# Kernel optimization log

Hardware: AMD Instinct MI355X
Metric: run time of the kernel (lower is better)

Reference implementation:

```python
import jax, jax.numpy as jnp
import numpy as np

K = 3            # pairwise_size
DIL = 2          # pairwise_dilation
COLOR_THR = 0.3  # pairwise_color_thresh
WARMUP = 1.0     # warmup factor (iter >= pairwise_warmup_iters)
COST_CLASS = 1.0
COST_PROJ = 1.0
COST_PAIR = 1.0


def unfold_wo_center(x, k, d):
    # x: (N, T, H, W) -> (N, T, k*k-1, H, W); neighbor at offset (i,j) with dilation d,
    # zero padding, center (i=j=k//2) removed, row-major order (matches F.unfold).
    pad = d * (k - 1) // 2
    H, W = x.shape[-2:]
    xp = jnp.pad(x, ((0, 0), (0, 0), (pad, pad), (pad, pad)))
    outs = []
    for i in range(k):
        for j in range(k):
            if i == k // 2 and j == k // 2:
                continue
            outs.append(xp[..., i * d:i * d + H, j * d:j * d + W])
    return jnp.stack(outs, axis=2)


def batch_dice_loss(inputs, targets):
    # inputs: (N, C), targets: (M, C)
    numerator = 2.0 * jnp.einsum('nc,mc->nm', inputs, targets)
    denominator = inputs.sum(-1)[:, None] + targets.sum(-1)[None, :]
    return 1.0 - (numerator + 1.0) / (denominator + 1.0)


def batch_axis_projection(out_mask, tgt_box_mask, axis):
    # max-project predicted (sigmoid) and box masks along `axis`, dice between projections
    src = jax.nn.sigmoid(out_mask).max(axis=axis).reshape(out_mask.shape[0], -1)
    tgt = tgt_box_mask.max(axis=axis).reshape(tgt_box_mask.shape[0], -1)
    return batch_dice_loss(src, tgt)


def calculate_similarity_cost_video(out_mask, tgt_box_mask, tgt_similarities):
    # out_mask: (Q,T,H,W); tgt_box_mask: (G,T,H,W); tgt_similarities: (G,T,8,H,W)
    Q, T = out_mask.shape[:2]
    G = tgt_box_mask.shape[0]
    tgt_sim = (tgt_similarities >= COLOR_THR).astype(jnp.float32) * tgt_box_mask[:, :, None]
    log_fg = jax.nn.log_sigmoid(out_mask)
    log_bg = jax.nn.log_sigmoid(-out_mask)
    log_fg_u = unfold_wo_center(log_fg, K, DIL)   # (Q,T,8,H,W)
    log_bg_u = unfold_wo_center(log_bg, K, DIL)
    # -log(exp(fg+fg_u) + exp(bg+bg_u)) computed stably
    src_sim = -jnp.logaddexp(log_fg[:, :, None] + log_fg_u,
                             log_bg[:, :, None] + log_bg_u)  # (Q,T,8,H,W)
    src_flat = src_sim.reshape(Q, T, -1)
    tgt_flat = tgt_sim.reshape(G, T, -1)
    numerator = jnp.einsum('qtc,gtc->tqg', src_flat, tgt_flat)      # (T,Q,G)
    denominator = jnp.clip(tgt_flat.sum(-1), 1.0, None)             # (G,T)
    cost = numerator / denominator.T[:, None, :]                    # (T,Q,G)
    return cost.mean(axis=0)                                        # (Q,G)


def setup_inputs() -> dict:
    key = jax.random.key(0)
    k1, k2, k3, k4, k5 = jax.random.split(key, 5)
    Q, G, T, H, W, C = 100, 16, 2, 128, 128, 81
    return {
        'pred_logits': jax.random.normal(k1, (Q, C), dtype=jnp.float32),
        'out_mask': jax.random.normal(k2, (Q, T, H, W), dtype=jnp.float32),
        'tgt_similarities': jax.random.uniform(k3, (G, T, K * K - 1, H, W), dtype=jnp.float32),
        'tgt_ids': jax.random.randint(k4, (G,), 0, C, dtype=jnp.int32),
        'tgt_box_mask': jax.random.randint(k5, (G, T, H, W), 0, 2, dtype=jnp.int32),
    }


def reference(pred_logits, out_mask, tgt_similarities, tgt_ids, tgt_box_mask):
    tgt_box_f = tgt_box_mask.astype(jnp.float32)
    out_prob = jax.nn.softmax(pred_logits, axis=-1)
    cost_class = -out_prob[:, tgt_ids]                                  # (Q,G)
    cost_projection = (batch_axis_projection(out_mask, tgt_box_f, 3)
                       + batch_axis_projection(out_mask, tgt_box_f, 2))  # (Q,G)
    cost_pairwise = calculate_similarity_cost_video(out_mask, tgt_box_f, tgt_similarities) * WARMUP
    C = COST_CLASS * cost_class + COST_PROJ * cost_projection + COST_PAIR * cost_pairwise
    return C
```

## Files before the change

kernel.cpp:

```cpp
#include <hip/hip_runtime.h>
#include <hip/hip_fp16.h>
#include <cstdint>

#define Q_ 100
#define G_ 16
#define T_ 2
#define H_ 128
#define W_ 128
#define HW_ (H_*W_)
#define C_ 81
#define RS_ 69
#define QS_ 553

typedef _Float16 half8 __attribute__((ext_vector_type(8)));
typedef float floatx4 __attribute__((ext_vector_type(4)));

__device__ __forceinline__ float sig_(float x) { return 1.0f / (1.0f + __expf(-x)); }

__launch_bounds__(256)
__global__ void k_srcmax(const float* __restrict__ om,
                         float* __restrict__ srcMW,
                         float* __restrict__ srcMHp) {
    int qt = blockIdx.x >> 2;
    int rg = blockIdx.x & 3;
    const float* base = om + (size_t)qt * HW_ + rg * 32 * W_;
    int tid = threadIdx.x;

    {
        int r = tid >> 3, seg = tid & 7;
        const float4* rp = (const float4*)(base + r * W_ + seg * 16);
        float m = -1e30f;
        #pragma unroll
        for (int i = 0; i < 4; ++i) {
            float4 v = rp[i];
            m = fmaxf(m, fmaxf(fmaxf(v.x, v.y), fmaxf(v.z, v.w)));
        }
        m = fmaxf(m, __shfl_xor(m, 1, 64));
        m = fmaxf(m, __shfl_xor(m, 2, 64));
        m = fmaxf(m, __shfl_xor(m, 4, 64));
        if (seg == 0) srcMW[qt * 128 + rg * 32 + r] = m;
    }
    __shared__ float cred[128];
    {
        int c = tid & 127, rh = tid >> 7;
        const float* cp = base + rh * 16 * W_ + c;
        float m = -1e30f;
        #pragma unroll
        for (int i = 0; i < 16; ++i) m = fmaxf(m, cp[i * W_]);
        if (rh == 1) cred[c] = m;
        __syncthreads();
        if (rh == 0) srcMHp[(qt * 4 + rg) * 128 + c] = fmaxf(m, cred[c]);
    }
}

__launch_bounds__(256)
__global__ void k_tgtmax(const int* __restrict__ box,
                         int* __restrict__ tgtMWi,
                         int* __restrict__ tgtMHp) {
    int gt = blockIdx.x >> 3;
    int rg = blockIdx.x & 7;
    const int* base = box + (size_t)gt * HW_ + rg * 16 * W_;
    int tid = threadIdx.x;
    {
        int r = tid >> 4, seg = tid & 15;
        const int4* rp = (const int4*)(base + r * W_ + seg * 8);
        int4 a = rp[0], b = rp[1];
        int m = max(max(max(a.x, a.y), max(a.z, a.w)),
                    max(max(b.x, b.y), max(b.z, b.w)));
        m = max(m, __shfl_xor(m, 1, 64));
        m = max(m, __shfl_xor(m, 2, 64));
        m = max(m, __shfl_xor(m, 4, 64));
        m = max(m, __shfl_xor(m, 8, 64));
        if (seg == 0) tgtMWi[gt * 128 + rg * 16 + r] = m;
    }
    __shared__ int credi[128];
    {
        int c = tid & 127, rh = tid >> 7;
        const int* cp = base + rh * 8 * W_ + c;
        int m = 0;
        #pragma unroll
        for (int i = 0; i < 8; ++i) m = max(m, cp[i * W_]);
        if (rh == 1) credi[c] = m;
        __syncthreads();
        if (rh == 0) tgtMHp[(gt * 8 + rg) * 128 + c] = max(m, credi[c]);
    }
}

__launch_bounds__(256)
__global__ void k_pack(const float* __restrict__ sims,
                       const int* __restrict__ box,
                       uint32_t* __restrict__ packed,
                       int* __restrict__ cnt_part) {
    int bid = blockIdx.x;
    int gg = bid & 3;
    int pxblk = bid >> 2;
    int tid = threadIdx.x;
    int p0 = pxblk * 512 + tid * 2;
    int t = p0 >> 14;
    int pp = p0 & (HW_ - 1);

    uint32_t w0 = 0, w1 = 0;
    int pc[4];
    #pragma unroll
    for (int b = 0; b < 4; ++b) {
        int g = gg * 4 + b;
        const float* sbase = sims + ((size_t)(g * T_ + t) * 8) * HW_ + pp;
        int2 bx = *(const int2*)(box + (size_t)(g * T_ + t) * HW_ + pp);
        uint32_t by0 = 0, by1 = 0;
        #pragma unroll
        for (int e = 0; e < 8; ++e) {
            float2 sv = *(const float2*)(sbase + (size_t)e * HW_);
            by0 |= (sv.x >= 0.3f ? 1u : 0u) << e;
            by1 |= (sv.y >= 0.3f ? 1u : 0u) << e;
        }
        by0 = bx.x ? by0 : 0u;
        by1 = bx.y ? by1 : 0u;
        w0 |= by0 << (b * 8);
        w1 |= by1 << (b * 8);
        pc[b] = __popc(by0) + __popc(by1);
    }
    *(uint2*)&packed[(size_t)gg * (T_ * HW_) + p0] = make_uint2(w0, w1);

    __shared__ int redI[4][4];
    int wid = tid >> 6, lane = tid & 63;
    #pragma unroll
    for (int b = 0; b < 4; ++b) {
        int s = pc[b];
        #pragma unroll
        for (int o = 32; o > 0; o >>= 1) s += __shfl_down(s, o, 64);
        if (lane == 0) redI[wid][b] = s;
    }
    __syncthreads();
    if (tid < 4)
        cnt_part[pxblk * 16 + gg * 4 + tid] =
            redI[0][tid] + redI[1][tid] + redI[2][tid] + redI[3][tid];
}

__global__ void k_dice(const float* __restrict__ logits, const int* __restrict__ ids,
                       const float* __restrict__ srcMW, const float* __restrict__ srcMHp,
                       const int* __restrict__ tgtMWi, const int* __restrict__ tgtMHp,
                       const int* __restrict__ cnt_part,
                       int* __restrict__ cntF,
                       float* __restrict__ out) {
    int q = blockIdx.x >> 4;
    int g = blockIdx.x & 15;
    int l = threadIdx.x;

    if (q == 0) {
        int tt = l >> 5, pb = l & 31;
        int v = cnt_part[(tt * 32 + pb) * 16 + g];
        #pragma unroll
        for (int o = 1; o <= 16; o <<= 1) v += __shfl_xor(v, o, 64);
        if (pb == 0) cntF[tt * G_ + g] = v;
    }

    float v0 = (l < C_) ? logits[q * C_ + l] : -1e30f;
    float v1 = (l + 64 < C_) ? logits[q * C_ + l + 64] : -1e30f;
    float mx = fmaxf(v0, v1);
    #pragma unroll
    for (int o = 32; o > 0; o >>= 1) mx = fmaxf(mx, __shfl_xor(mx, o, 64));
    float es = ((l < C_) ? __expf(v0 - mx) : 0.0f)
             + ((l + 64 < C_) ? __expf(v1 - mx) : 0.0f);
    #pragma unroll
    for (int o = 32; o > 0; o >>= 1) es += __shfl_xor(es, o, 64);

    float d3 = 0, t3 = 0, s3 = 0, d2 = 0, t2 = 0, s2 = 0;
    #pragma unroll
    for (int i = 0; i < 4; ++i) {
        int c = i * 64 + l;
        int tt = c >> 7, cc = c & 127;
        float sW = sig_(srcMW[(q * 2 + tt) * 128 + cc]);
        float mh = srcMHp[((q * 2 + tt) * 4 + 0) * 128 + cc];
        #pragma unroll
        for (int r = 1; r < 4; ++r)
            mh = fmaxf(mh, srcMHp[((q * 2 + tt) * 4 + r) * 128 + cc]);
        float sH = sig_(mh);
        float tW = (float)tgtMWi[(g * 2 + tt) * 128 + cc];
        int th = tgtMHp[((g * 2 + tt) * 8 + 0) * 128 + cc];
        #pragma unroll
        for (int r = 1; r < 8; ++r)
            th = max(th, tgtMHp[((g * 2 + tt) * 8 + r) * 128 + cc]);
        float tH = (float)th;
        d3 += sW * tW; t3 += tW; s3 += sW;
        d2 += sH * tH; t2 += tH; s2 += sH;
    }
    #pragma unroll
    for (int o = 32; o > 0; o >>= 1) {
        d3 += __shfl_xor(d3, o, 64); t3 += __shfl_xor(t3, o, 64);
        s3 += __shfl_xor(s3, o, 64); d2 += __shfl_xor(d2, o, 64);
        t2 += __shfl_xor(t2, o, 64); s2 += __shfl_xor(s2, o, 64);
    }
    if (l == 0) {
        float p = __expf(logits[q * C_ + ids[g]] - mx) / es;
        float dice3 = 1.0f - (2.0f * d3 + 1.0f) / (s3 + t3 + 1.0f);
        float dice2 = 1.0f - (2.0f * d2 + 1.0f) / (s2 + t2 + 1.0f);
        out[q * G_ + g] = -p + dice3 + dice2;
    }
}

__launch_bounds__(256, 4)
__global__ void k_pair(const float* __restrict__ om,
                       const uint32_t* __restrict__ packed,
                       const int* __restrict__ cntF,
                       float* __restrict__ out) {
    int bid = blockIdx.x;
    int wh = bid & 1;
    int rg = (bid >> 1) & 31;
    int t  = (bid >> 6) & 1;
    int qt = bid >> 7;
    int qbase = qt * 16;
    int rowbase = rg * 4;
    int cbase = wh * 64;
    int tid = threadIdx.x;

    __shared__ uint32_t tile[16 * QS_];

    #pragma unroll
    for (int i = 0; i < 8; ++i) {
        int idx = i * 256 + tid;
        int c4 = idx & 15;
        int row = (idx >> 4) & 7;
        int q = idx >> 7;
        int gq = qbase + q;
        int grow = rowbase - 2 + row;
        float4 x = make_float4(0.f, 0.f, 0.f, 0.f);
        if (gq < Q_ && (unsigned)grow < (unsigned)H_)
            x = *(const float4*)(om + (((size_t)gq * T_ + t) * H_ + grow) * W_ + cbase + c4 * 4);
        uint32_t* dst = &tile[q * QS_ + row * RS_ + 2 + c4 * 4];
        {
            float E = __expf(-x.x); __half2 h = __floats2half2_rn(E, __logf(1.f + E)); dst[0] = *(uint32_t*)&h;
        }{
            float E = __expf(-x.y); __half2 h = __floats2half2_rn(E, __logf(1.f + E)); dst[1] = *(uint32_t*)&h;
        }{
            float E = __expf(-x.z); __half2 h = __floats2half2_rn(E, __logf(1.f + E)); dst[2] = *(uint32_t*)&h;
        }{
            float E = __expf(-x.w); __half2 h = __floats2half2_rn(E, __logf(1.f + E)); dst[3] = *(uint32_t*)&h;
        }
    }
    #pragma unroll
    for (int i = 0; i < 2; ++i) {
        int idx = i * 256 + tid;
        int cc = idx & 3;
        int row = (idx >> 2) & 7;
        int q = idx >> 5;
        int col = (cc < 2) ? cc : cc + 64;
        int gcol = cbase - 2 + col;
        int gq = qbase + q;
        int grow = rowbase - 2 + row;
        float x = 0.f;
        if (gq < Q_ && (unsigned)grow < (unsigned)H_ && (unsigned)gcol < (unsigned)W_)
            x = om[(((size_t)gq * T_ + t) * H_ + grow) * W_ + gcol];
        float E = __expf(-x);
        __half2 h = __floats2half2_rn(E, __logf(1.f + E));
        tile[q * QS_ + row * RS_ + col] = *(uint32_t*)&h;
    }
    __syncthreads();

    int l = tid & 63;
    int w = tid >> 6;
    int mn = l & 15;
    int pq = l >> 4;
    int growS = rowbase + w;

    const uint32_t* pbase = packed + (size_t)(mn >> 2) * (T_ * HW_) + t * HW_
                          + (growS << 7) + cbase + (pq << 4);
    uint4 pkA = *(const uint4*)(pbase + 0);
    uint4 pkB = *(const uint4*)(pbase + 4);
    uint4 pkC = *(const uint4*)(pbase + 8);
    uint4 pkD = *(const uint4*)(pbase + 12);
    uint32_t pkw[16] = {pkA.x, pkA.y, pkA.z, pkA.w, pkB.x, pkB.y, pkB.z, pkB.w,
                        pkC.x, pkC.y, pkC.z, pkC.w, pkD.x, pkD.y, pkD.z, pkD.w};

    const uint32_t* tq = &tile[mn * QS_ + (w + 2) * RS_ + 2 + (pq << 4)];

    bool rowU = (growS >= 2), rowD = (growS <= H_ - 3);
    int bsh = (mn & 3) * 8;

    const int dy[8] = {-2,-2,-2, 0,0, 2,2,2};
    const int dx[8] = {-2, 0, 2,-2,2,-2,0,2};

    floatx4 acc0 = {0.f,0.f,0.f,0.f}, acc1 = {0.f,0.f,0.f,0.f};

    #pragma unroll
    for (int grp = 0; grp < 16; ++grp) {
        int gcol = cbase + (pq << 4) + grp;
        bool colL = (gcol >= 2), colR = (gcol <= W_ - 3);
        bool m8[8] = {rowU && colL, rowU, rowU && colR,
                      colL, colR,
                      rowD && colL, rowD, rowD && colR};

        uint32_t selfw = tq[grp];
        __half2 sh = *(__half2*)&selfw;
        float Ep = __half2float(__low2half(sh));
        float Lp = __half2float(__high2half(sh));
        uint32_t byte = (pkw[grp] >> bsh) & 255u;

        half8 af, bf;
        #pragma unroll
        for (int e = 0; e < 8; ++e) {
            uint32_t nw = tq[grp + dy[e] * RS_ + dx[e]];
            __half2 nh = *(__half2*)&nw;
            float En = __half2float(__low2half(nh));
            float Ln = __half2float(__high2half(nh));
            float s = Lp + Ln - __logf(fmaf(Ep, En, 1.0f));
            s = m8[e] ? s : 0.0f;
            af[e] = (_Float16)s;
            bf[e] = (_Float16)(float)((byte >> e) & 1u);
        }
        if (grp & 1) acc1 = __builtin_amdgcn_mfma_f32_16x16x32_f16(af, bf, acc1, 0, 0, 0);
        else         acc0 = __builtin_amdgcn_mfma_f32_16x16x32_f16(af, bf, acc0, 0, 0, 0);
    }

    __syncthreads();
    float* red = (float*)tile;
    #pragma unroll
    for (int j = 0; j < 4; ++j)
        red[(w * 16 + pq * 4 + j) * 17 + mn] = acc0[j] + acc1[j];
    __syncthreads();
    {
        int row = tid >> 4, g = tid & 15;
        float v = red[(0 * 16 + row) * 17 + g] + red[(1 * 16 + row) * 17 + g]
                + red[(2 * 16 + row) * 17 + g] + red[(3 * 16 + row) * 17 + g];
        int gq = qbase + row;
        if (gq < Q_) {
            int den = max(1, cntF[t * G_ + g]);
            atomicAdd(&out[gq * G_ + g], v * (0.5f / (float)den));
        }
    }
}

extern "C" void kernel_launch(void* const* d_in, const int* in_sizes, int n_in,
                              void* d_out, int out_size, void* d_ws, size_t ws_size,
                              hipStream_t stream) {
    const float* pred_logits = (const float*)d_in[0];
    const float* out_mask    = (const float*)d_in[1];
    const float* sims        = (const float*)d_in[2];
    const int*   tgt_ids     = (const int*)d_in[3];
    const int*   tgt_box     = (const int*)d_in[4];
    float* out = (float*)d_out;

    float*    srcMW    = (float*)d_ws;
    float*    srcMHp   = srcMW + Q_ * T_ * 128;
    int*      tgtMWi   = (int*)(srcMHp + Q_ * T_ * 4 * 128);
    int*      tgtMHp   = tgtMWi + G_ * T_ * 128;
    int*      cnt_part = tgtMHp + G_ * T_ * 8 * 128;
    int*      cntF     = cnt_part + 64 * 16;
    uint32_t* packed   = (uint32_t*)(cntF + G_ * T_);

    k_srcmax<<<Q_ * T_ * 4, 256, 0, stream>>>(out_mask, srcMW, srcMHp);
    k_tgtmax<<<G_ * T_ * 8, 256, 0, stream>>>(tgt_box, tgtMWi, tgtMHp);
    k_pack<<<(T_ * HW_ / 512) * 4, 256, 0, stream>>>(sims, tgt_box, packed, cnt_part);
    k_dice<<<Q_ * G_, 64, 0, stream>>>(pred_logits, tgt_ids, srcMW, srcMHp,
                                       tgtMWi, tgtMHp, cnt_part, cntF, out);
    k_pair<<<7 * T_ * 32 * 2, 256, 0, stream>>>(out_mask, packed, cntF, out);
}
```

Before: 122.2 us.

## Merge three prep kernels into one launch and build MFMA B operand via bit tricks

Merges k_srcmax, k_tgtmax and k_pack into a single k_prep kernel that dispatches on block index ranges. This removes two kernel launches and lets the independent prep work overlap across CUs. Separately, in k_pair the 0/1 half-precision B operand is now built with integer bit tricks (multiplying the isolated bits by the fp16 encoding of 1.0) instead of per-element int-to-float-to-half conversions. Shared memory is reused across the branches; the merged kernel keeps the same per-branch work.

```diff
diff --git a/kernel.cpp b/kernel.cpp
--- a/kernel.cpp
+++ b/kernel.cpp
@@ -18,122 +18,119 @@
 __device__ __forceinline__ float sig_(float x) { return 1.0f / (1.0f + __expf(-x)); }
 
 __launch_bounds__(256)
-__global__ void k_srcmax(const float* __restrict__ om,
-                         float* __restrict__ srcMW,
-                         float* __restrict__ srcMHp) {
-    int qt = blockIdx.x >> 2;
-    int rg = blockIdx.x & 3;
-    const float* base = om + (size_t)qt * HW_ + rg * 32 * W_;
-    int tid = threadIdx.x;
-
-    {
-        int r = tid >> 3, seg = tid & 7;
-        const float4* rp = (const float4*)(base + r * W_ + seg * 16);
-        float m = -1e30f;
-        #pragma unroll
-        for (int i = 0; i < 4; ++i) {
-            float4 v = rp[i];
-            m = fmaxf(m, fmaxf(fmaxf(v.x, v.y), fmaxf(v.z, v.w)));
-        }
-        m = fmaxf(m, __shfl_xor(m, 1, 64));
-        m = fmaxf(m, __shfl_xor(m, 2, 64));
-        m = fmaxf(m, __shfl_xor(m, 4, 64));
-        if (seg == 0) srcMW[qt * 128 + rg * 32 + r] = m;
-    }
-    __shared__ float cred[128];
-    {
-        int c = tid & 127, rh = tid >> 7;
-        const float* cp = base + rh * 16 * W_ + c;
-        float m = -1e30f;
-        #pragma unroll
-        for (int i = 0; i < 16; ++i) m = fmaxf(m, cp[i * W_]);
-        if (rh == 1) cred[c] = m;
-        __syncthreads();
-        if (rh == 0) srcMHp[(qt * 4 + rg) * 128 + c] = fmaxf(m, cred[c]);
-    }
-}
-
-__launch_bounds__(256)
-__global__ void k_tgtmax(const int* __restrict__ box,
-                         int* __restrict__ tgtMWi,
-                         int* __restrict__ tgtMHp) {
-    int gt = blockIdx.x >> 3;
-    int rg = blockIdx.x & 7;
-    const int* base = box + (size_t)gt * HW_ + rg * 16 * W_;
-    int tid = threadIdx.x;
-    {
-        int r = tid >> 4, seg = tid & 15;
-        const int4* rp = (const int4*)(base + r * W_ + seg * 8);
-        int4 a = rp[0], b = rp[1];
-        int m = max(max(max(a.x, a.y), max(a.z, a.w)),
-                    max(max(b.x, b.y), max(b.z, b.w)));
-        m = max(m, __shfl_xor(m, 1, 64));
-        m = max(m, __shfl_xor(m, 2, 64));
-        m = max(m, __shfl_xor(m, 4, 64));
-        m = max(m, __shfl_xor(m, 8, 64));
-        if (seg == 0) tgtMWi[gt * 128 + rg * 16 + r] = m;
-    }
-    __shared__ int credi[128];
-    {
-        int c = tid & 127, rh = tid >> 7;
-        const int* cp = base + rh * 8 * W_ + c;
-        int m = 0;
-        #pragma unroll
-        for (int i = 0; i < 8; ++i) m = max(m, cp[i * W_]);
-        if (rh == 1) credi[c] = m;
-        __syncthreads();
-        if (rh == 0) tgtMHp[(gt * 8 + rg) * 128 + c] = max(m, credi[c]);
-    }
-}
-
-__launch_bounds__(256)
-__global__ void k_pack(const float* __restrict__ sims,
+__global__ void k_prep(const float* __restrict__ om,
                        const int* __restrict__ box,
+                       const float* __restrict__ sims,
+                       float* __restrict__ srcMW,
+                       float* __restrict__ srcMHp,
+                       int* __restrict__ tgtMWi,
+                       int* __restrict__ tgtMHp,
                        uint32_t* __restrict__ packed,
                        int* __restrict__ cnt_part) {
+    __shared__ float credF[128];
+    __shared__ int redI[4][4];
     int bid = blockIdx.x;
-    int gg = bid & 3;
-    int pxblk = bid >> 2;
     int tid = threadIdx.x;
-    int p0 = pxblk * 512 + tid * 2;
-    int t = p0 >> 14;
-    int pp = p0 & (HW_ - 1);
-
-    uint32_t w0 = 0, w1 = 0;
-    int pc[4];
-    #pragma unroll
-    for (int b = 0; b < 4; ++b) {
-        int g = gg * 4 + b;
-        const float* sbase = sims + ((size_t)(g * T_ + t) * 8) * HW_ + pp;
-        int2 bx = *(const int2*)(box + (size_t)(g * T_ + t) * HW_ + pp);
-        uint32_t by0 = 0, by1 = 0;
-        #pragma unroll
-        for (int e = 0; e < 8; ++e) {
-            float2 sv = *(const float2*)(sbase + (size_t)e * HW_);
-            by0 |= (sv.x >= 0.3f ? 1u : 0u) << e;
-            by1 |= (sv.y >= 0.3f ? 1u : 0u) << e;
-        }
-        by0 = bx.x ? by0 : 0u;
-        by1 = bx.y ? by1 : 0u;
-        w0 |= by0 << (b * 8);
-        w1 |= by1 << (b * 8);
-        pc[b] = __popc(by0) + __popc(by1);
-    }
-    *(uint2*)&packed[(size_t)gg * (T_ * HW_) + p0] = make_uint2(w0, w1);
-
-    __shared__ int redI[4][4];
-    int wid = tid >> 6, lane = tid & 63;
-    #pragma unroll
-    for (int b = 0; b < 4; ++b) {
-        int s = pc[b];
-        #pragma unroll
-        for (int o = 32; o > 0; o >>= 1) s += __shfl_down(s, o, 64);
-        if (lane == 0) redI[wid][b] = s;
-    }
-    __syncthreads();
-    if (tid < 4)
-        cnt_part[pxblk * 16 + gg * 4 + tid] =
-            redI[0][tid] + redI[1][tid] + redI[2][tid] + redI[3][tid];
+
+    if (bid < 800) {
+        int qt = bid >> 2;
+        int rg = bid & 3;
+        const float* base = om + (size_t)qt * HW_ + rg * 32 * W_;
+        {
+            int r = tid >> 3, seg = tid & 7;
+            const float4* rp = (const float4*)(base + r * W_ + seg * 16);
+            float m = -1e30f;
+            #pragma unroll
+            for (int i = 0; i < 4; ++i) {
+                float4 v = rp[i];
+                m = fmaxf(m, fmaxf(fmaxf(v.x, v.y), fmaxf(v.z, v.w)));
+            }
+            m = fmaxf(m, __shfl_xor(m, 1, 64));
+            m = fmaxf(m, __shfl_xor(m, 2, 64));
+            m = fmaxf(m, __shfl_xor(m, 4, 64));
+            if (seg == 0) srcMW[qt * 128 + rg * 32 + r] = m;
+        }
+        {
+            int c = tid & 127, rh = tid >> 7;
+            const float* cp = base + rh * 16 * W_ + c;
+            float m = -1e30f;
+            #pragma unroll
+            for (int i = 0; i < 16; ++i) m = fmaxf(m, cp[i * W_]);
+            if (rh == 1) credF[c] = m;
+            __syncthreads();
+            if (rh == 0) srcMHp[(qt * 4 + rg) * 128 + c] = fmaxf(m, credF[c]);
+        }
+    } else if (bid < 1056) {
+        int b2 = bid - 800;
+        int gt = b2 >> 3;
+        int rg = b2 & 7;
+        const int* base = box + (size_t)gt * HW_ + rg * 16 * W_;
+        {
+            int r = tid >> 4, seg = tid & 15;
+            const int4* rp = (const int4*)(base + r * W_ + seg * 8);
+            int4 a = rp[0], b = rp[1];
+            int m = max(max(max(a.x, a.y), max(a.z, a.w)),
+                        max(max(b.x, b.y), max(b.z, b.w)));
+            m = max(m, __shfl_xor(m, 1, 64));
+            m = max(m, __shfl_xor(m, 2, 64));
+            m = max(m, __shfl_xor(m, 4, 64));
+            m = max(m, __shfl_xor(m, 8, 64));
+            if (seg == 0) tgtMWi[gt * 128 + rg * 16 + r] = m;
+        }
+        {
+            int* credi = (int*)credF;
+            int c = tid & 127, rh = tid >> 7;
+            const int* cp = base + rh * 8 * W_ + c;
+            int m = 0;
+            #pragma unroll
+            for (int i = 0; i < 8; ++i) m = max(m, cp[i * W_]);
+            if (rh == 1) credi[c] = m;
+            __syncthreads();
+            if (rh == 0) tgtMHp[(gt * 8 + rg) * 128 + c] = max(m, credi[c]);
+        }
+    } else {
+        int b3 = bid - 1056;
+        int gg = b3 & 3;
+        int pxblk = b3 >> 2;
+        int p0 = pxblk * 512 + tid * 2;
+        int t = p0 >> 14;
+        int pp = p0 & (HW_ - 1);
+
+        uint32_t w0 = 0, w1 = 0;
+        int pc[4];
+        #pragma unroll
+        for (int b = 0; b < 4; ++b) {
+            int g = gg * 4 + b;
+            const float* sbase = sims + ((size_t)(g * T_ + t) * 8) * HW_ + pp;
+            int2 bx = *(const int2*)(box + (size_t)(g * T_ + t) * HW_ + pp);
+            uint32_t by0 = 0, by1 = 0;
+            #pragma unroll
+            for (int e = 0; e < 8; ++e) {
+                float2 sv = *(const float2*)(sbase + (size_t)e * HW_);
+                by0 |= (sv.x >= 0.3f ? 1u : 0u) << e;
+                by1 |= (sv.y >= 0.3f ? 1u : 0u) << e;
+            }
+            by0 = bx.x ? by0 : 0u;
+            by1 = bx.y ? by1 : 0u;
+            w0 |= by0 << (b * 8);
+            w1 |= by1 << (b * 8);
+            pc[b] = __popc(by0) + __popc(by1);
+        }
+        *(uint2*)&packed[(size_t)gg * (T_ * HW_) + p0] = make_uint2(w0, w1);
+
+        int wid = tid >> 6, lane = tid & 63;
+        #pragma unroll
+        for (int b = 0; b < 4; ++b) {
+            int s = pc[b];
+            #pragma unroll
+            for (int o = 32; o > 0; o >>= 1) s += __shfl_down(s, o, 64);
+            if (lane == 0) redI[wid][b] = s;
+        }
+        __syncthreads();
+        if (tid < 4)
+            cnt_part[pxblk * 16 + gg * 4 + tid] =
+                redI[0][tid] + redI[1][tid] + redI[2][tid] + redI[3][tid];
+    }
 }
 
 __global__ void k_dice(const float* __restrict__ logits, const int* __restrict__ ids,
@@ -295,7 +292,7 @@
         float Lp = __half2float(__high2half(sh));
         uint32_t byte = (pkw[grp] >> bsh) & 255u;
 
-        half8 af, bf;
+        half8 af;
         #pragma unroll
         for (int e = 0; e < 8; ++e) {
             uint32_t nw = tq[grp + dy[e] * RS_ + dx[e]];
@@ -305,10 +302,16 @@
             float s = Lp + Ln - __logf(fmaf(Ep, En, 1.0f));
             s = m8[e] ? s : 0.0f;
             af[e] = (_Float16)s;
-            bf[e] = (_Float16)(float)((byte >> e) & 1u);
-        }
-        if (grp & 1) acc1 = __builtin_amdgcn_mfma_f32_16x16x32_f16(af, bf, acc1, 0, 0, 0);
-        else         acc0 = __builtin_amdgcn_mfma_f32_16x16x32_f16(af, bf, acc0, 0, 0, 0);
+        }
+        union { half8 h; uint32_t w4[4]; } bfu;
+        uint32_t xb = byte | (byte << 15);
+        bfu.w4[0] = ((xb >> 0) & 0x10001u) * 0x3C00u;
+        bfu.w4[1] = ((xb >> 2) & 0x10001u) * 0x3C00u;
+        bfu.w4[2] = ((xb >> 4) & 0x10001u) * 0x3C00u;
+        bfu.w4[3] = ((xb >> 6) & 0x10001u) * 0x3C00u;
+
+        if (grp & 1) acc1 = __builtin_amdgcn_mfma_f32_16x16x32_f16(af, bfu.h, acc1, 0, 0, 0);
+        else         acc0 = __builtin_amdgcn_mfma_f32_16x16x32_f16(af, bfu.h, acc0, 0, 0, 0);
     }
 
     __syncthreads();
@@ -347,9 +350,8 @@
     int*      cntF     = cnt_part + 64 * 16;
     uint32_t* packed   = (uint32_t*)(cntF + G_ * T_);
 
-    k_srcmax<<<Q_ * T_ * 4, 256, 0, stream>>>(out_mask, srcMW, srcMHp);
-    k_tgtmax<<<G_ * T_ * 8, 256, 0, stream>>>(tgt_box, tgtMWi, tgtMHp);
-    k_pack<<<(T_ * HW_ / 512) * 4, 256, 0, stream>>>(sims, tgt_box, packed, cnt_part);
+    k_prep<<<1312, 256, 0, stream>>>(out_mask, tgt_box, sims,
+                                     srcMW, srcMHp, tgtMWi, tgtMHp, packed, cnt_part);
     k_dice<<<Q_ * G_, 64, 0, stream>>>(pred_logits, tgt_ids, srcMW, srcMHp,
                                        tgtMWi, tgtMHp, cnt_part, cntF, out);
     k_pair<<<7 * T_ * 32 * 2, 256, 0, stream>>>(out_mask, packed, cntF, out);
```

After: 113.0 us. 1.08x faster.
